# Optimization experiments

Hardware: AMD Instinct MI355X
Metric: run time of the kernel (lower is better)

## Reference

```python
import jax, jax.numpy as jnp
import numpy as np

D = 128
H = 4
B = 4096
K = 64
N_USERS = 200000
BISECT_ITERS = 50


def l2norm(x, axis=-1, eps=1e-12):
    n = jnp.linalg.norm(x, axis=axis, keepdims=True)
    return x / jnp.maximum(n, eps)


def entmax_bisect(x, alpha, n_iter=BISECT_ITERS):
    # x, alpha: [B, K, 1]; entmax normalization over the neighbor axis (axis=1)
    # p = max((alpha-1)*x - tau, 0)**(1/(alpha-1)) with tau found by bisection so sum_k p = 1
    am1 = alpha - 1.0            # in (0,1) since alpha = sigmoid(.)+1
    q = 1.0 / am1                # exponent > 1, so p is smooth at 0
    xs = x * am1
    mx = jnp.max(xs, axis=1, keepdims=True)
    tau_lo = mx - 1.0            # f(tau_lo) >= 0
    tau_hi = mx                  # f(tau_hi) <= 0

    def p_of(tau):
        t = jnp.maximum(xs - tau, 0.0)
        safe = jnp.where(t > 0.0, t, 1.0)
        return jnp.where(t > 0.0, safe ** q, 0.0)

    def body(i, carry):
        lo, hi = carry
        mid = 0.5 * (lo + hi)
        f_m = jnp.sum(p_of(mid), axis=1, keepdims=True) - 1.0
        lo = jnp.where(f_m >= 0.0, mid, lo)
        hi = jnp.where(f_m >= 0.0, hi, mid)
        return (lo, hi)

    tau_lo, tau_hi = jax.lax.fori_loop(0, n_iter, body, (tau_lo, tau_hi))
    p = p_of(0.5 * (tau_lo + tau_hi))
    return p / jnp.sum(p, axis=1, keepdims=True)


def batchnorm(x, g, b, eps=1e-5):
    # training-mode BatchNorm1d: batch statistics, biased variance
    m = jnp.mean(x, axis=0)
    v = jnp.mean((x - m) ** 2, axis=0)
    return (x - m) * jax.lax.rsqrt(v + eps) * g + b


def setup_inputs() -> dict:
    key = jax.random.key(0)
    ks = jax.random.split(key, 16)
    s = 0.05
    return {
        'nodes': jax.random.randint(ks[0], (B,), 0, N_USERS),
        'neighbors': jax.random.randint(ks[1], (B, K), 0, N_USERS),
        'u2e': jax.random.normal(ks[2], (N_USERS, D), jnp.float32),
        'att1_w': jax.random.normal(ks[3], (H, 2 * D, D), jnp.float32) * s,
        'att1_b': jnp.zeros((H, D), jnp.float32),
        'att2_w': jax.random.normal(ks[4], (H, D, D // 4), jnp.float32) * s,
        'att2_b': jnp.zeros((H, D // 4), jnp.float32),
        'att3_w': jax.random.normal(ks[5], (H, D // 4, 1), jnp.float32) * s,
        'att3_b': jnp.zeros((H, 1), jnp.float32),
        'lin1_w': jax.random.normal(ks[6], (H, D, 1), jnp.float32) * s,
        'lin1_b': jnp.zeros((H, 1), jnp.float32),
        'gate_w': jax.random.normal(ks[7], (3 * D, D), jnp.float32) * s,
        'gate_b': jnp.zeros((D,), jnp.float32),
        'bn_g': jnp.ones((D,), jnp.float32),
        'bn_b': jnp.zeros((D,), jnp.float32),
        'bn1_g': jnp.ones((D,), jnp.float32),
        'bn1_b': jnp.zeros((D,), jnp.float32),
        'in_w': jax.random.normal(ks[8], (D, D), jnp.float32) * s,
        'in_b': jnp.zeros((D,), jnp.float32),
        'out_w': jax.random.normal(ks[9], (D, D), jnp.float32) * s,
        'out_b': jnp.zeros((D,), jnp.float32),
    }


def reference(nodes, neighbors, u2e, att1_w, att1_b, att2_w, att2_b, att3_w,
              att3_b, lin1_w, lin1_b, gate_w, gate_b, bn_g, bn_b, bn1_g,
              bn1_b, in_w, in_b, out_w, out_b):
    n_heads = att1_w.shape[0]
    e_n = l2norm(u2e[neighbors])                     # [B,K,D] normalized neighbor embeds
    u = u2e[nodes]                                   # [B,D]
    b, k, d = e_n.shape
    feats = []
    for h in range(n_heads):
        u_n = l2norm(u)
        x = jnp.concatenate(
            [e_n, jnp.broadcast_to(u_n[:, None, :], (b, k, d))], axis=-1)
        alpha = jax.nn.sigmoid(e_n @ lin1_w[h] + lin1_b[h]) + 1.0  # [B,K,1]
        sc = jax.nn.selu(x @ att1_w[h] + att1_b[h])
        sc = jax.nn.selu(sc @ att2_w[h] + att2_b[h])
        sc = sc @ att3_w[h] + att3_b[h]                            # [B,K,1]
        att = entmax_bisect(sc, alpha)                             # [B,K,1]
        u = jnp.einsum('bkd,bk->bd', e_n, att[..., 0])             # weighted pool
        feats.append(u)
    att_hist = sum(feats) / n_heads                  # [B,D]
    # GAT_MLP (dropout omitted: eval)
    h1 = batchnorm(att_hist, bn_g, bn_b)
    h1 = jax.nn.selu(h1 @ in_w + in_b)
    h1 = batchnorm(h1, bn1_g, bn1_b)
    neigh = h1 @ out_w + out_b                       # [B,D]
    self_f = u2e[nodes]
    comb = jnp.concatenate([self_f, neigh, self_f * neigh], axis=-1)
    gama = jax.nn.sigmoid(comb @ gate_w + gate_b)
    return gama * self_f + (1.0 - gama) * neigh
```

## Files before the change

### kernel.cpp

```cpp
#include <hip/hip_runtime.h>
#include <stdint.h>

#define NB 4096
#define NK 64
#define ND 128
#define NH 4
#define ES 136
#define ESW (ES/2)
#define FS 130
#define MR 8

typedef __attribute__((ext_vector_type(8))) short bf16x8;
typedef __attribute__((ext_vector_type(4))) float f32x4;

__device__ __forceinline__ float seluf(float x) {
    float e = 1.6732632423543772f * (__expf(x) - 1.f);
    return 1.0507009873554805f * (x > 0.f ? x : e);
}
__device__ __forceinline__ float sigmoidf_(float x) {
    return __fdividef(1.f, 1.f + __expf(-x));
}
__device__ __forceinline__ uint32_t f2bf2(float a, float b) {
    uint32_t ua = __float_as_uint(a); ua += 0x7fffu + ((ua >> 16) & 1u);
    uint32_t ub = __float_as_uint(b); ub += 0x7fffu + ((ub >> 16) & 1u);
    return (ua >> 16) | (ub & 0xffff0000u);
}
__device__ __forceinline__ uint16_t bf1(float v) {
    uint32_t u = __float_as_uint(v); u += 0x7fffu + ((u >> 16) & 1u);
    return (uint16_t)(u >> 16);
}
__device__ __forceinline__ float bflo(uint32_t v) { return __uint_as_float(v << 16); }
__device__ __forceinline__ float bfhi(uint32_t v) { return __uint_as_float(v & 0xffff0000u); }
__device__ __forceinline__ float bf2f(uint16_t h) { return __uint_as_float(((uint32_t)h) << 16); }

__global__ __launch_bounds__(256)
void k_prep(const float* __restrict__ att1_w, const float* __restrict__ att2_w,
            uint16_t* __restrict__ wt1, uint16_t* __restrict__ wt2)
{
    const int h = blockIdx.x >> 2;
    const int q = blockIdx.x & 3;
    const int t = threadIdx.x;
    {
        int n = t >> 1, kh = t & 1;
        for (int k0 = q * 16; k0 < q * 16 + 16; ++k0) {
            int k = k0 * 2 + kh;
            float v = att1_w[(size_t)h * 32768 + (size_t)k * ND + n];
            float vo = __shfl_xor(v, 1, 64);
            if (kh == 0)
                ((uint32_t*)wt1)[((size_t)h * ND + n) * 64 + k0] = f2bf2(v, vo);
        }
    }
    {
        int c = t & 31, dh = t >> 5;
        for (int d0 = q * 4; d0 < q * 4 + 4; ++d0) {
            int d = d0 * 8 + dh;
            float v = att2_w[(size_t)h * 4096 + (size_t)d * 32 + c];
            float vo = __shfl_xor(v, 32, 64);
            if ((dh & 1) == 0)
                ((uint32_t*)wt2)[((size_t)h * 32 + c) * 64 + d0 * 4 + (dh >> 1)] = f2bf2(v, vo);
        }
    }
}

__global__ __launch_bounds__(256, 4)
void k_att(const int* __restrict__ nodes, const int* __restrict__ neighbors,
           const float* __restrict__ u2e,
           const float* __restrict__ att1_w, const float* __restrict__ att1_b,
           const float* __restrict__ att2_b,
           const float* __restrict__ att3_w, const float* __restrict__ att3_b,
           const float* __restrict__ lin1_w, const float* __restrict__ lin1_b,
           const uint16_t* __restrict__ wt1, const uint16_t* __restrict__ wt2,
           float* __restrict__ hist_out,
           float* __restrict__ sums, float* __restrict__ sumsq)
{
    __shared__ alignas(16) uint16_t e_sh[NK * ES];
    __shared__ alignas(16) uint16_t s1_sh[NK * ES];
    __shared__ float u_sh[ND], un_sh[ND], up_sh[ND], lw_sh[ND], hist_sh[ND];
    __shared__ float alpha_sh[NK], sc_sh[NK], att_sh[NK];
    __shared__ float red_sh[512];
    __shared__ float rnorm_sh;

    const int b = blockIdx.x;
    const int t = threadIdx.x;
    const int lane = t & 63;
    const int wave = t >> 6;
    const int lh = lane & 15;
    const int lg = lane >> 4;

    for (int k = wave; k < NK; k += 4) {
        int idx = neighbors[b * NK + k];
        float2 v = ((const float2*)(u2e + (size_t)idx * ND))[lane];
        float ss = v.x * v.x + v.y * v.y;
        #pragma unroll
        for (int m = 1; m < 64; m <<= 1) ss += __shfl_xor(ss, m, 64);
        float r = 1.0f / fmaxf(sqrtf(ss), 1e-12f);
        ((uint32_t*)e_sh)[k * ESW + lane] = f2bf2(v.x * r, v.y * r);
    }
    if (t < ND) {
        u_sh[t] = u2e[(size_t)nodes[b] * ND + t];
        hist_sh[t] = 0.f;
    }
    __syncthreads();

    for (int h = 0; h < NH; ++h) {
        if (wave == 0) {
            float a = u_sh[lane], c = u_sh[lane + 64];
            float ss = a * a + c * c;
            #pragma unroll
            for (int m = 1; m < 64; m <<= 1) ss += __shfl_xor(ss, m, 64);
            if (lane == 0) rnorm_sh = 1.0f / fmaxf(sqrtf(ss), 1e-12f);
        }
        __syncthreads();
        if (t < ND) {
            un_sh[t] = u_sh[t] * rnorm_sh;
            lw_sh[t] = lin1_w[h * ND + t];
        }
        __syncthreads();

        {
            int d = t & 127, half = t >> 7;
            const float* wb = att1_w + (size_t)h * 32768 + (size_t)(ND + half * 64) * ND + d;
            float p = 0.f;
            #pragma unroll 8
            for (int j = 0; j < 64; ++j)
                p += un_sh[half * 64 + j] * wb[j * ND];
            red_sh[t] = p;
        }
        {
            int k = t >> 2, qd = t & 3;
            const uint32_t* er = (const uint32_t*)e_sh + k * ESW + qd * 16;
            const float* lr = lw_sh + qd * 32;
            float ap = 0.f;
            #pragma unroll 8
            for (int j2 = 0; j2 < 16; ++j2) {
                uint32_t v = er[j2];
                ap += bflo(v) * lr[2 * j2] + bfhi(v) * lr[2 * j2 + 1];
            }
            ap += __shfl_xor(ap, 1, 64);
            ap += __shfl_xor(ap, 2, 64);
            if (qd == 0)
                alpha_sh[k] = sigmoidf_(ap + lin1_b[h]) + 1.0f;
        }
        __syncthreads();
        if (t < ND)
            up_sh[t] = red_sh[t] + red_sh[t + 128] + att1_b[h * ND + t];
        __syncthreads();

        {
            const uint16_t* WB = wt1 + ((size_t)h * ND + wave * 32) * ND;
            bf16x8 B[4][2];
            #pragma unroll
            for (int kk = 0; kk < 4; ++kk)
                #pragma unroll
                for (int nt = 0; nt < 2; ++nt)
                    B[kk][nt] = *(const bf16x8*)(WB + (nt * 16 + lh) * ND + kk * 32 + lg * 8);
            f32x4 z = {0.f, 0.f, 0.f, 0.f};
            f32x4 acc[4][2] = {{z, z}, {z, z}, {z, z}, {z, z}};
            #pragma unroll
            for (int mt = 0; mt < 4; ++mt) {
                #pragma unroll
                for (int kk = 0; kk < 4; ++kk) {
                    bf16x8 A = *(const bf16x8*)(e_sh + (mt * 16 + lh) * ES + kk * 32 + lg * 8);
                    acc[mt][0] = __builtin_amdgcn_mfma_f32_16x16x32_bf16(A, B[kk][0], acc[mt][0], 0, 0, 0);
                    acc[mt][1] = __builtin_amdgcn_mfma_f32_16x16x32_bf16(A, B[kk][1], acc[mt][1], 0, 0, 0);
                }
            }
            float up0 = up_sh[wave * 32 + lh];
            float up1 = up_sh[wave * 32 + 16 + lh];
            #pragma unroll
            for (int mt = 0; mt < 4; ++mt)
                #pragma unroll
                for (int nt = 0; nt < 2; ++nt) {
                    float upv = nt ? up1 : up0;
                    #pragma unroll
                    for (int r = 0; r < 4; ++r) {
                        float v = seluf(acc[mt][nt][r] + upv);
                        s1_sh[(mt * 16 + lg * 4 + r) * ES + wave * 32 + nt * 16 + lh] = bf1(v);
                    }
                }
        }
        __syncthreads();

        {
            const uint16_t* WB2 = wt2 + (size_t)h * 32 * ND;
            bf16x8 B2[4][2];
            #pragma unroll
            for (int kk = 0; kk < 4; ++kk)
                #pragma unroll
                for (int nt = 0; nt < 2; ++nt)
                    B2[kk][nt] = *(const bf16x8*)(WB2 + (nt * 16 + lh) * ND + kk * 32 + lg * 8);
            f32x4 z = {0.f, 0.f, 0.f, 0.f};
            f32x4 acc2[2] = {z, z};
            #pragma unroll
            for (int kk = 0; kk < 4; ++kk) {
                bf16x8 A = *(const bf16x8*)(s1_sh + (wave * 16 + lh) * ES + kk * 32 + lg * 8);
                acc2[0] = __builtin_amdgcn_mfma_f32_16x16x32_bf16(A, B2[kk][0], acc2[0], 0, 0, 0);
                acc2[1] = __builtin_amdgcn_mfma_f32_16x16x32_bf16(A, B2[kk][1], acc2[1], 0, 0, 0);
            }
            float w3a = att3_w[h * 32 + lh],      b2a = att2_b[h * 32 + lh];
            float w3b = att3_w[h * 32 + 16 + lh], b2b = att2_b[h * 32 + 16 + lh];
            float b3 = att3_b[h];
            #pragma unroll
            for (int r = 0; r < 4; ++r) {
                float v = seluf(acc2[0][r] + b2a) * w3a + seluf(acc2[1][r] + b2b) * w3b;
                v += __shfl_xor(v, 1, 64);
                v += __shfl_xor(v, 2, 64);
                v += __shfl_xor(v, 4, 64);
                v += __shfl_xor(v, 8, 64);
                if (lh == 0)
                    sc_sh[wave * 16 + lg * 4 + r] = v + b3;
            }
        }
        __syncthreads();

        if (wave == 0) {
            float x   = sc_sh[lane];
            float am1 = alpha_sh[lane] - 1.0f;
            float q   = 1.0f / am1;
            float em1 = q - 1.0f;
            float xs  = x * am1;
            float mx = xs;
            #pragma unroll
            for (int m = 1; m < 64; m <<= 1) mx = fmaxf(mx, __shfl_xor(mx, m, 64));
            float tau = mx - 1.0f;
            for (int it = 0; it < 8; ++it) {
                float tt = xs - tau;
                bool pos = tt > 0.f;
                float lgn = __logf(pos ? tt : 1.f);
                float p  = pos ? __expf(q * lgn) : 0.f;
                float dp = pos ? q * __expf(em1 * lgn) : 0.f;
                float s0 = p, s1 = dp;
                #pragma unroll
                for (int m = 1; m < 64; m <<= 1) {
                    s0 += __shfl_xor(s0, m, 64);
                    s1 += __shfl_xor(s1, m, 64);
                }
                tau += __fdividef(s0 - 1.0f, fmaxf(s1, 1e-30f));
                tau = fminf(tau, mx - 1e-6f);
            }
            float tt = xs - tau;
            bool pos = tt > 0.f;
            float p = pos ? __expf(q * __logf(pos ? tt : 1.f)) : 0.f;
            float s0 = p;
            #pragma unroll
            for (int m = 1; m < 64; m <<= 1) s0 += __shfl_xor(s0, m, 64);
            att_sh[lane] = __fdividef(p, s0);
        }
        __syncthreads();

        {
            int d2 = t & 63, qk = t >> 6;
            const uint32_t* E = (const uint32_t*)e_sh;
            float px = 0.f, py = 0.f;
            #pragma unroll 8
            for (int k = qk * 16; k < qk * 16 + 16; ++k) {
                uint32_t v = E[k * ESW + d2];
                float a = att_sh[k];
                px += bflo(v) * a;
                py += bfhi(v) * a;
            }
            red_sh[qk * 128 + d2 * 2]     = px;
            red_sh[qk * 128 + d2 * 2 + 1] = py;
        }
        __syncthreads();
        if (t < ND) {
            float un = red_sh[t] + red_sh[128 + t] + red_sh[256 + t] + red_sh[384 + t];
            u_sh[t] = un;
            hist_sh[t] += un;
        }
        __syncthreads();
    }
    if (t < ND) {
        float hv = hist_sh[t] * 0.25f;
        hist_out[(size_t)b * ND + t] = hv;
        atomicAdd(&sums[t], hv);
        atomicAdd(&sumsq[t], hv * hv);
    }
}

__global__ __launch_bounds__(256)
void k_mlp1(const float* __restrict__ hist,
            const float* __restrict__ sums, const float* __restrict__ sumsq,
            const float* __restrict__ bn_g, const float* __restrict__ bn_b,
            const float* __restrict__ in_w, const float* __restrict__ in_b,
            float* __restrict__ h1out,
            float* __restrict__ sums1, float* __restrict__ sumsq1)
{
    __shared__ float xh[MR * FS];
    int t = threadIdx.x;
    int row0 = blockIdx.x * MR;
    for (int i = t; i < MR * ND; i += 256) {
        int r = i >> 7, d = i & 127;
        float m  = sums[d]  * (1.f / 4096.f);
        float vv = sumsq[d] * (1.f / 4096.f) - m * m;
        float sc = bn_g[d] * rsqrtf(vv + 1e-5f);
        float sh = bn_b[d] - m * sc;
        xh[r * FS + d] = hist[(size_t)(row0 + r) * ND + d] * sc + sh;
    }
    __syncthreads();
    int dg = t & 31, rg = t >> 5;
    int d0 = dg * 4;
    float acc[4] = {};
    for (int j = 0; j < ND; ++j) {
        float4 wa = *(const float4*)(in_w + (size_t)j * ND + d0);
        float e = xh[rg * FS + j];
        acc[0] += e * wa.x; acc[1] += e * wa.y;
        acc[2] += e * wa.z; acc[3] += e * wa.w;
    }
    float hv[4];
    #pragma unroll
    for (int c = 0; c < 4; ++c) {
        hv[c] = seluf(acc[c] + in_b[d0 + c]);
        h1out[(size_t)(row0 + rg) * ND + d0 + c] = hv[c];
    }
    __syncthreads();
    #pragma unroll
    for (int c = 0; c < 4; ++c) xh[rg * FS + d0 + c] = hv[c];
    __syncthreads();
    if (t < ND) {
        float s = 0.f, q = 0.f;
        #pragma unroll
        for (int r = 0; r < MR; ++r) {
            float v = xh[r * FS + t];
            s += v; q += v * v;
        }
        atomicAdd(&sums1[t], s);
        atomicAdd(&sumsq1[t], q);
    }
}

__global__ __launch_bounds__(256)
void k_final(const float* __restrict__ h1,
             const float* __restrict__ sums1, const float* __restrict__ sumsq1,
             const float* __restrict__ bn1_g, const float* __restrict__ bn1_b,
             const float* __restrict__ out_w, const float* __restrict__ out_b,
             const float* __restrict__ gate_w, const float* __restrict__ gate_b,
             const int* __restrict__ nodes, const float* __restrict__ u2e,
             float* __restrict__ out)
{
    __shared__ float xh[MR * FS];
    __shared__ float sf[MR * FS];
    __shared__ float ng[MR * FS];
    int t = threadIdx.x;
    int row0 = blockIdx.x * MR;
    for (int i = t; i < MR * ND; i += 256) {
        int r = i >> 7, d = i & 127;
        float m  = sums1[d]  * (1.f / 4096.f);
        float vv = sumsq1[d] * (1.f / 4096.f) - m * m;
        float sc = bn1_g[d] * rsqrtf(vv + 1e-5f);
        float sh = bn1_b[d] - m * sc;
        xh[r * FS + d] = h1[(size_t)(row0 + r) * ND + d] * sc + sh;
        sf[r * FS + d] = u2e[(size_t)nodes[row0 + r] * ND + d];
    }
    __syncthreads();
    int dg = t & 31, rg = t >> 5;
    int d0 = dg * 4;
    {
        float acc[4] = {};
        for (int j = 0; j < ND; ++j) {
            float4 wa = *(const float4*)(out_w + (size_t)j * ND + d0);
            float e = xh[rg * FS + j];
            acc[0] += e * wa.x; acc[1] += e * wa.y;
            acc[2] += e * wa.z; acc[3] += e * wa.w;
        }
        #pragma unroll
        for (int c = 0; c < 4; ++c)
            ng[rg * FS + d0 + c] = acc[c] + out_b[d0 + c];
    }
    __syncthreads();
    {
        float acc[4] = {};
        for (int j = 0; j < ND; ++j) {
            float4 w0 = *(const float4*)(gate_w + (size_t)j * ND + d0);
            float4 w1 = *(const float4*)(gate_w + (size_t)(ND + j) * ND + d0);
            float4 w2 = *(const float4*)(gate_w + (size_t)(2 * ND + j) * ND + d0);
            float s = sf[rg * FS + j];
            float n = ng[rg * FS + j];
            float p = s * n;
            acc[0] += s * w0.x + n * w1.x + p * w2.x;
            acc[1] += s * w0.y + n * w1.y + p * w2.y;
            acc[2] += s * w0.z + n * w1.z + p * w2.z;
            acc[3] += s * w0.w + n * w1.w + p * w2.w;
        }
        #pragma unroll
        for (int c = 0; c < 4; ++c) {
            int d = d0 + c;
            float gama = sigmoidf_(acc[c] + gate_b[d]);
            float s = sf[rg * FS + d];
            float n = ng[rg * FS + d];
            out[(size_t)(row0 + rg) * ND + d] = gama * s + (1.f - gama) * n;
        }
    }
}

extern "C" void kernel_launch(void* const* d_in, const int* in_sizes, int n_in,
                              void* d_out, int out_size, void* d_ws, size_t ws_size,
                              hipStream_t stream)
{
    const int*   nodes     = (const int*)d_in[0];
    const int*   neighbors = (const int*)d_in[1];
    const float* u2e       = (const float*)d_in[2];
    const float* att1_w    = (const float*)d_in[3];
    const float* att1_b    = (const float*)d_in[4];
    const float* att2_w    = (const float*)d_in[5];
    const float* att2_b    = (const float*)d_in[6];
    const float* att3_w    = (const float*)d_in[7];
    const float* att3_b    = (const float*)d_in[8];
    const float* lin1_w    = (const float*)d_in[9];
    const float* lin1_b    = (const float*)d_in[10];
    const float* gate_w    = (const float*)d_in[11];
    const float* gate_b    = (const float*)d_in[12];
    const float* bn_g      = (const float*)d_in[13];
    const float* bn_b      = (const float*)d_in[14];
    const float* bn1_g     = (const float*)d_in[15];
    const float* bn1_b     = (const float*)d_in[16];
    const float* in_w      = (const float*)d_in[17];
    const float* in_b      = (const float*)d_in[18];
    const float* out_w     = (const float*)d_in[19];
    const float* out_b     = (const float*)d_in[20];
    float* out = (float*)d_out;

    float* ws     = (float*)d_ws;
    float* g_hist = ws;
    float* h1     = ws + (size_t)NB * ND;
    float* st     = ws + (size_t)2 * NB * ND;
    uint16_t* wt1 = (uint16_t*)(ws + (size_t)2 * NB * ND + 512);
    uint16_t* wt2 = wt1 + (size_t)NH * ND * ND;

    (void)hipMemsetAsync(st, 0, 512 * sizeof(float), stream);

    k_prep<<<16, 256, 0, stream>>>(att1_w, att2_w, wt1, wt2);
    k_att<<<NB, 256, 0, stream>>>(nodes, neighbors, u2e,
                                  att1_w, att1_b, att2_b,
                                  att3_w, att3_b, lin1_w, lin1_b,
                                  wt1, wt2,
                                  g_hist, st, st + 128);
    k_mlp1<<<NB / MR, 256, 0, stream>>>(g_hist, st, st + 128, bn_g, bn_b,
                                        in_w, in_b, h1, st + 256, st + 384);
    k_final<<<NB / MR, 256, 0, stream>>>(h1, st + 256, st + 384, bn1_g, bn1_b,
                                         out_w, out_b, gate_w, gate_b,
                                         nodes, u2e, out);
}
```

Baseline: 559.0 us.

## Restructure attention kernel per-wave rows, hoist alpha, reduce Newton iters, widen MLP grids

Alpha (the lin1 gate) is now computed for all four heads up front, with one head per wave, instead of once per head inside the loop. The per-head rnorm is computed redundantly in every wave, which removes two barriers. The first MFMA GEMM now gives each wave 16 rows and all 128 columns, so the second GEMM reads only that wave's own s1 slice and the barrier between the two GEMMs goes away. The entmax Newton iterations drop from 8 to 6, and the MLP kernels use MR=4 with 2 outputs per thread for more blocks. The trade-offs are that B fragments are now reloaded from global memory, and fewer iterations may reduce numerical accuracy.

Result: slower. 780.2 us (+39.6%).

```diff
diff --git a/kernel.cpp b/kernel.cpp
--- a/kernel.cpp
+++ b/kernel.cpp
@@ -8,7 +8,7 @@
 #define ES 136
 #define ESW (ES/2)
 #define FS 130
-#define MR 8
+#define MR 4
 
 typedef __attribute__((ext_vector_type(8))) short bf16x8;
 typedef __attribute__((ext_vector_type(4))) float f32x4;
@@ -31,18 +31,17 @@
 }
 __device__ __forceinline__ float bflo(uint32_t v) { return __uint_as_float(v << 16); }
 __device__ __forceinline__ float bfhi(uint32_t v) { return __uint_as_float(v & 0xffff0000u); }
-__device__ __forceinline__ float bf2f(uint16_t h) { return __uint_as_float(((uint32_t)h) << 16); }
 
 __global__ __launch_bounds__(256)
 void k_prep(const float* __restrict__ att1_w, const float* __restrict__ att2_w,
             uint16_t* __restrict__ wt1, uint16_t* __restrict__ wt2)
 {
-    const int h = blockIdx.x >> 2;
-    const int q = blockIdx.x & 3;
+    const int h = blockIdx.x >> 4;
+    const int q = blockIdx.x & 15;
     const int t = threadIdx.x;
     {
         int n = t >> 1, kh = t & 1;
-        for (int k0 = q * 16; k0 < q * 16 + 16; ++k0) {
+        for (int k0 = q * 4; k0 < q * 4 + 4; ++k0) {
             int k = k0 * 2 + kh;
             float v = att1_w[(size_t)h * 32768 + (size_t)k * ND + n];
             float vo = __shfl_xor(v, 1, 64);
@@ -52,13 +51,12 @@
     }
     {
         int c = t & 31, dh = t >> 5;
-        for (int d0 = q * 4; d0 < q * 4 + 4; ++d0) {
-            int d = d0 * 8 + dh;
-            float v = att2_w[(size_t)h * 4096 + (size_t)d * 32 + c];
-            float vo = __shfl_xor(v, 32, 64);
-            if ((dh & 1) == 0)
-                ((uint32_t*)wt2)[((size_t)h * 32 + c) * 64 + d0 * 4 + (dh >> 1)] = f2bf2(v, vo);
-        }
+        int d0 = q;
+        int d = d0 * 8 + dh;
+        float v = att2_w[(size_t)h * 4096 + (size_t)d * 32 + c];
+        float vo = __shfl_xor(v, 32, 64);
+        if ((dh & 1) == 0)
+            ((uint32_t*)wt2)[((size_t)h * 32 + c) * 64 + d0 * 4 + (dh >> 1)] = f2bf2(v, vo);
     }
 }
 
@@ -75,10 +73,10 @@
 {
     __shared__ alignas(16) uint16_t e_sh[NK * ES];
     __shared__ alignas(16) uint16_t s1_sh[NK * ES];
-    __shared__ float u_sh[ND], un_sh[ND], up_sh[ND], lw_sh[ND], hist_sh[ND];
-    __shared__ float alpha_sh[NK], sc_sh[NK], att_sh[NK];
+    __shared__ float u_sh[ND], up_sh[ND], hist_sh[ND];
+    __shared__ float alpha_sh[NH * NK];
+    __shared__ float sc_sh[NK], att_sh[NK];
     __shared__ float red_sh[512];
-    __shared__ float rnorm_sh;
 
     const int b = blockIdx.x;
     const int t = threadIdx.x;
@@ -102,100 +100,87 @@
     }
     __syncthreads();
 
+    {
+        const float* lw = lin1_w + wave * ND;
+        float lb = lin1_b[wave];
+        #pragma unroll
+        for (int it = 0; it < 4; ++it) {
+            int k = it * 16 + (lane >> 2);
+            int qd = lane & 3;
+            const uint32_t* er = (const uint32_t*)e_sh + k * ESW + qd * 16;
+            const float* lr = lw + qd * 32;
+            float ap = 0.f;
+            #pragma unroll 8
+            for (int j2 = 0; j2 < 16; ++j2) {
+                uint32_t v = er[j2];
+                ap += bflo(v) * lr[2 * j2] + bfhi(v) * lr[2 * j2 + 1];
+            }
+            ap += __shfl_xor(ap, 1, 64);
+            ap += __shfl_xor(ap, 2, 64);
+            if (qd == 0)
+                alpha_sh[wave * NK + k] = sigmoidf_(ap + lb) + 1.0f;
+        }
+    }
+
     for (int h = 0; h < NH; ++h) {
-        if (wave == 0) {
+        float rnorm;
+        {
             float a = u_sh[lane], c = u_sh[lane + 64];
             float ss = a * a + c * c;
             #pragma unroll
             for (int m = 1; m < 64; m <<= 1) ss += __shfl_xor(ss, m, 64);
-            if (lane == 0) rnorm_sh = 1.0f / fmaxf(sqrtf(ss), 1e-12f);
-        }
-        __syncthreads();
-        if (t < ND) {
-            un_sh[t] = u_sh[t] * rnorm_sh;
-            lw_sh[t] = lin1_w[h * ND + t];
-        }
-        __syncthreads();
-
+            rnorm = 1.0f / fmaxf(sqrtf(ss), 1e-12f);
+        }
         {
             int d = t & 127, half = t >> 7;
             const float* wb = att1_w + (size_t)h * 32768 + (size_t)(ND + half * 64) * ND + d;
             float p = 0.f;
             #pragma unroll 8
             for (int j = 0; j < 64; ++j)
-                p += un_sh[half * 64 + j] * wb[j * ND];
-            red_sh[t] = p;
-        }
-        {
-            int k = t >> 2, qd = t & 3;
-            const uint32_t* er = (const uint32_t*)e_sh + k * ESW + qd * 16;
-            const float* lr = lw_sh + qd * 32;
-            float ap = 0.f;
-            #pragma unroll 8
-            for (int j2 = 0; j2 < 16; ++j2) {
-                uint32_t v = er[j2];
-                ap += bflo(v) * lr[2 * j2] + bfhi(v) * lr[2 * j2 + 1];
-            }
-            ap += __shfl_xor(ap, 1, 64);
-            ap += __shfl_xor(ap, 2, 64);
-            if (qd == 0)
-                alpha_sh[k] = sigmoidf_(ap + lin1_b[h]) + 1.0f;
+                p += u_sh[half * 64 + j] * wb[j * ND];
+            red_sh[t] = p * rnorm;
         }
         __syncthreads();
         if (t < ND)
             up_sh[t] = red_sh[t] + red_sh[t + 128] + att1_b[h * ND + t];
         __syncthreads();
 
+        uint16_t* s1w = s1_sh + wave * 16 * ES;
         {
-            const uint16_t* WB = wt1 + ((size_t)h * ND + wave * 32) * ND;
-            bf16x8 B[4][2];
-            #pragma unroll
-            for (int kk = 0; kk < 4; ++kk)
+            const uint16_t* WB = wt1 + (size_t)h * ND * ND;
+            f32x4 z = {0.f, 0.f, 0.f, 0.f};
+            f32x4 acc[8] = {z, z, z, z, z, z, z, z};
+            #pragma unroll
+            for (int kk = 0; kk < 4; ++kk) {
+                bf16x8 A = *(const bf16x8*)(e_sh + (wave * 16 + lh) * ES + kk * 32 + lg * 8);
                 #pragma unroll
-                for (int nt = 0; nt < 2; ++nt)
-                    B[kk][nt] = *(const bf16x8*)(WB + (nt * 16 + lh) * ND + kk * 32 + lg * 8);
+                for (int nt = 0; nt < 8; ++nt) {
+                    bf16x8 Bf = *(const bf16x8*)(WB + (size_t)(nt * 16 + lh) * ND + kk * 32 + lg * 8);
+                    acc[nt] = __builtin_amdgcn_mfma_f32_16x16x32_bf16(A, Bf, acc[nt], 0, 0, 0);
+                }
+            }
+            #pragma unroll
+            for (int nt = 0; nt < 8; ++nt) {
+                float upv = up_sh[nt * 16 + lh];
+                #pragma unroll
+                for (int r = 0; r < 4; ++r) {
+                    float v = seluf(acc[nt][r] + upv);
+                    s1w[(lg * 4 + r) * ES + nt * 16 + lh] = bf1(v);
+                }
+            }
+        }
+        {
+            const uint16_t* WB2 = wt2 + (size_t)h * 32 * ND;
             f32x4 z = {0.f, 0.f, 0.f, 0.f};
-            f32x4 acc[4][2] = {{z, z}, {z, z}, {z, z}, {z, z}};
-            #pragma unroll
-            for (int mt = 0; mt < 4; ++mt) {
-                #pragma unroll
-                for (int kk = 0; kk < 4; ++kk) {
-                    bf16x8 A = *(const bf16x8*)(e_sh + (mt * 16 + lh) * ES + kk * 32 + lg * 8);
-                    acc[mt][0] = __builtin_amdgcn_mfma_f32_16x16x32_bf16(A, B[kk][0], acc[mt][0], 0, 0, 0);
-                    acc[mt][1] = __builtin_amdgcn_mfma_f32_16x16x32_bf16(A, B[kk][1], acc[mt][1], 0, 0, 0);
-                }
-            }
-            float up0 = up_sh[wave * 32 + lh];
-            float up1 = up_sh[wave * 32 + 16 + lh];
-            #pragma unroll
-            for (int mt = 0; mt < 4; ++mt)
+            f32x4 acc2[2] = {z, z};
+            #pragma unroll
+            for (int kk = 0; kk < 4; ++kk) {
+                bf16x8 A = *(const bf16x8*)(s1w + lh * ES + kk * 32 + lg * 8);
                 #pragma unroll
                 for (int nt = 0; nt < 2; ++nt) {
-                    float upv = nt ? up1 : up0;
-                    #pragma unroll
-                    for (int r = 0; r < 4; ++r) {
-                        float v = seluf(acc[mt][nt][r] + upv);
-                        s1_sh[(mt * 16 + lg * 4 + r) * ES + wave * 32 + nt * 16 + lh] = bf1(v);
-                    }
+                    bf16x8 Bf = *(const bf16x8*)(WB2 + (size_t)(nt * 16 + lh) * ND + kk * 32 + lg * 8);
+                    acc2[nt] = __builtin_amdgcn_mfma_f32_16x16x32_bf16(A, Bf, acc2[nt], 0, 0, 0);
                 }
-        }
-        __syncthreads();
-
-        {
-            const uint16_t* WB2 = wt2 + (size_t)h * 32 * ND;
-            bf16x8 B2[4][2];
-            #pragma unroll
-            for (int kk = 0; kk < 4; ++kk)
-                #pragma unroll
-                for (int nt = 0; nt < 2; ++nt)
-                    B2[kk][nt] = *(const bf16x8*)(WB2 + (nt * 16 + lh) * ND + kk * 32 + lg * 8);
-            f32x4 z = {0.f, 0.f, 0.f, 0.f};
-            f32x4 acc2[2] = {z, z};
-            #pragma unroll
-            for (int kk = 0; kk < 4; ++kk) {
-                bf16x8 A = *(const bf16x8*)(s1_sh + (wave * 16 + lh) * ES + kk * 32 + lg * 8);
-                acc2[0] = __builtin_amdgcn_mfma_f32_16x16x32_bf16(A, B2[kk][0], acc2[0], 0, 0, 0);
-                acc2[1] = __builtin_amdgcn_mfma_f32_16x16x32_bf16(A, B2[kk][1], acc2[1], 0, 0, 0);
             }
             float w3a = att3_w[h * 32 + lh],      b2a = att2_b[h * 32 + lh];
             float w3b = att3_w[h * 32 + 16 + lh], b2b = att2_b[h * 32 + 16 + lh];
@@ -215,7 +200,7 @@
 
         if (wave == 0) {
             float x   = sc_sh[lane];
-            float am1 = alpha_sh[lane] - 1.0f;
+            float am1 = alpha_sh[h * NK + lane] - 1.0f;
             float q   = 1.0f / am1;
             float em1 = q - 1.0f;
             float xs  = x * am1;
@@ -223,7 +208,7 @@
             #pragma unroll
             for (int m = 1; m < 64; m <<= 1) mx = fmaxf(mx, __shfl_xor(mx, m, 64));
             float tau = mx - 1.0f;
-            for (int it = 0; it < 8; ++it) {
+            for (int it = 0; it < 6; ++it) {
                 float tt = xs - tau;
                 bool pos = tt > 0.f;
                 float lgn = __logf(pos ? tt : 1.f);
@@ -298,24 +283,22 @@
         xh[r * FS + d] = hist[(size_t)(row0 + r) * ND + d] * sc + sh;
     }
     __syncthreads();
-    int dg = t & 31, rg = t >> 5;
-    int d0 = dg * 4;
-    float acc[4] = {};
+    int dg = t & 63, rg = t >> 6;
+    int d0 = dg * 2;
+    float a0 = 0.f, a1 = 0.f;
+    #pragma unroll 4
     for (int j = 0; j < ND; ++j) {
-        float4 wa = *(const float4*)(in_w + (size_t)j * ND + d0);
+        float2 w = *(const float2*)(in_w + (size_t)j * ND + d0);
         float e = xh[rg * FS + j];
-        acc[0] += e * wa.x; acc[1] += e * wa.y;
-        acc[2] += e * wa.z; acc[3] += e * wa.w;
-    }
-    float hv[4];
-    #pragma unroll
-    for (int c = 0; c < 4; ++c) {
-        hv[c] = seluf(acc[c] + in_b[d0 + c]);
-        h1out[(size_t)(row0 + rg) * ND + d0 + c] = hv[c];
-    }
-    __syncthreads();
-    #pragma unroll
-    for (int c = 0; c < 4; ++c) xh[rg * FS + d0 + c] = hv[c];
+        a0 += e * w.x; a1 += e * w.y;
+    }
+    float h0 = seluf(a0 + in_b[d0]);
+    float h1v = seluf(a1 + in_b[d0 + 1]);
+    h1out[(size_t)(row0 + rg) * ND + d0]     = h0;
+    h1out[(size_t)(row0 + rg) * ND + d0 + 1] = h1v;
+    __syncthreads();
+    xh[rg * FS + d0] = h0;
+    xh[rg * FS + d0 + 1] = h1v;
     __syncthreads();
     if (t < ND) {
         float s = 0.f, q = 0.f;
@@ -353,39 +336,38 @@
         sf[r * FS + d] = u2e[(size_t)nodes[row0 + r] * ND + d];
     }
     __syncthreads();
-    int dg = t & 31, rg = t >> 5;
-    int d0 = dg * 4;
+    int dg = t & 63, rg = t >> 6;
+    int d0 = dg * 2;
     {
-        float acc[4] = {};
+        float a0 = 0.f, a1 = 0.f;
+        #pragma unroll 4
         for (int j = 0; j < ND; ++j) {
-            float4 wa = *(const float4*)(out_w + (size_t)j * ND + d0);
+            float2 w = *(const float2*)(out_w + (size_t)j * ND + d0);
             float e = xh[rg * FS + j];
-            acc[0] += e * wa.x; acc[1] += e * wa.y;
-            acc[2] += e * wa.z; acc[3] += e * wa.w;
-        }
-        #pragma unroll
-        for (int c = 0; c < 4; ++c)
-            ng[rg * FS + d0 + c] = acc[c] + out_b[d0 + c];
+            a0 += e * w.x; a1 += e * w.y;
+        }
+        ng[rg * FS + d0]     = a0 + out_b[d0];
+        ng[rg * FS + d0 + 1] = a1 + out_b[d0 + 1];
     }
     __syncthreads();
     {
-        float acc[4] = {};
+        float a0 = 0.f, a1 = 0.f;
+        #pragma unroll 2
         for (int j = 0; j < ND; ++j) {
-            float4 w0 = *(const float4*)(gate_w + (size_t)j * ND + d0);
-            float4 w1 = *(const float4*)(gate_w + (size_t)(ND + j) * ND + d0);
-            float4 w2 = *(const float4*)(gate_w + (size_t)(2 * ND + j) * ND + d0);
+            float2 w0 = *(const float2*)(gate_w + (size_t)j * ND + d0);
+            float2 w1 = *(const float2*)(gate_w + (size_t)(ND + j) * ND + d0);
+            float2 w2 = *(const float2*)(gate_w + (size_t)(2 * ND + j) * ND + d0);
             float s = sf[rg * FS + j];
             float n = ng[rg * FS + j];
             float p = s * n;
-            acc[0] += s * w0.x + n * w1.x + p * w2.x;
-            acc[1] += s * w0.y + n * w1.y + p * w2.y;
-            acc[2] += s * w0.z + n * w1.z + p * w2.z;
-            acc[3] += s * w0.w + n * w1.w + p * w2.w;
+            a0 += s * w0.x + n * w1.x + p * w2.x;
+            a1 += s * w0.y + n * w1.y + p * w2.y;
         }
         #pragma unroll
-        for (int c = 0; c < 4; ++c) {
+        for (int c = 0; c < 2; ++c) {
             int d = d0 + c;
-            float gama = sigmoidf_(acc[c] + gate_b[d]);
+            float acc = c ? a1 : a0;
+            float gama = sigmoidf_(acc + gate_b[d]);
             float s = sf[rg * FS + d];
             float n = ng[rg * FS + d];
             out[(size_t)(row0 + rg) * ND + d] = gama * s + (1.f - gama) * n;
@@ -429,7 +411,7 @@
 
     (void)hipMemsetAsync(st, 0, 512 * sizeof(float), stream);
 
-    k_prep<<<16, 256, 0, stream>>>(att1_w, att2_w, wt1, wt2);
+    k_prep<<<64, 256, 0, stream>>>(att1_w, att2_w, wt1, wt2);
     k_att<<<NB, 256, 0, stream>>>(nodes, neighbors, u2e,
                                   att1_w, att1_b, att2_b,
                                   att3_w, att3_b, lin1_w, lin1_b,
```

## Move MLP and gate GEMMs to bf16 MFMA and hoist alpha computation

Applied to the files above, without the earlier changes.

The MLP and gate weights are pre-transposed to bf16 in the prep kernel, and the in/out/gate matmuls in k_mlp1 and k_final become 16x16x32 bf16 MFMA tiles with 16 rows per block. The intermediate h1 is stored as bf16. In k_att, the per-head alpha computation is hoisted out of the head loop, the u normalisation is folded into a per-wave scale, removing two barriers per head, and the entmax Newton iterations drop from 8 to 6. The aim is to replace scalar FP32 FMA loops and cut syncs and traffic, at the cost of bf16 precision in the MLP and possibly less converged entmax.

New measurement: 526.0 us. -5.9%, faster.

```diff
diff --git a/kernel.cpp b/kernel.cpp
--- a/kernel.cpp
+++ b/kernel.cpp
@@ -7,8 +7,9 @@
 #define NH 4
 #define ES 136
 #define ESW (ES/2)
-#define FS 130
-#define MR 8
+#define MR 16
+#define GS 392
+#define SFS 132
 
 typedef __attribute__((ext_vector_type(8))) short bf16x8;
 typedef __attribute__((ext_vector_type(4))) float f32x4;
@@ -35,30 +36,51 @@
 
 __global__ __launch_bounds__(256)
 void k_prep(const float* __restrict__ att1_w, const float* __restrict__ att2_w,
-            uint16_t* __restrict__ wt1, uint16_t* __restrict__ wt2)
+            const float* __restrict__ in_w, const float* __restrict__ out_w,
+            const float* __restrict__ gate_w,
+            uint16_t* __restrict__ wt1, uint16_t* __restrict__ wt2,
+            uint16_t* __restrict__ wt_in, uint16_t* __restrict__ wt_out,
+            uint16_t* __restrict__ wt_gate)
 {
-    const int h = blockIdx.x >> 2;
-    const int q = blockIdx.x & 3;
+    const int bx = blockIdx.x;
     const int t = threadIdx.x;
-    {
-        int n = t >> 1, kh = t & 1;
-        for (int k0 = q * 16; k0 < q * 16 + 16; ++k0) {
-            int k = k0 * 2 + kh;
-            float v = att1_w[(size_t)h * 32768 + (size_t)k * ND + n];
-            float vo = __shfl_xor(v, 1, 64);
-            if (kh == 0)
-                ((uint32_t*)wt1)[((size_t)h * ND + n) * 64 + k0] = f2bf2(v, vo);
-        }
-    }
-    {
-        int c = t & 31, dh = t >> 5;
-        for (int d0 = q * 4; d0 < q * 4 + 4; ++d0) {
+    if (bx < 64) {
+        const int h = bx >> 4;
+        const int q = bx & 15;
+        {
+            int n = t >> 1, kh = t & 1;
+            for (int k0 = q * 4; k0 < q * 4 + 4; ++k0) {
+                int k = k0 * 2 + kh;
+                float v = att1_w[(size_t)h * 32768 + (size_t)k * ND + n];
+                float vo = __shfl_xor(v, 1, 64);
+                if (kh == 0)
+                    ((uint32_t*)wt1)[((size_t)h * ND + n) * 64 + k0] = f2bf2(v, vo);
+            }
+        }
+        {
+            int c = t & 31, dh = t >> 5;
+            int d0 = q;
             int d = d0 * 8 + dh;
             float v = att2_w[(size_t)h * 4096 + (size_t)d * 32 + c];
             float vo = __shfl_xor(v, 32, 64);
             if ((dh & 1) == 0)
                 ((uint32_t*)wt2)[((size_t)h * 32 + c) * 64 + d0 * 4 + (dh >> 1)] = f2bf2(v, vo);
         }
+    } else if (bx < 72) {
+        int n0 = (bx - 64) * 16;
+        for (int n = n0; n < n0 + 16; ++n)
+            for (int k = t; k < ND; k += 256)
+                wt_in[n * ND + k] = bf1(in_w[(size_t)k * ND + n]);
+    } else if (bx < 80) {
+        int n0 = (bx - 72) * 16;
+        for (int n = n0; n < n0 + 16; ++n)
+            for (int k = t; k < ND; k += 256)
+                wt_out[n * ND + k] = bf1(out_w[(size_t)k * ND + n]);
+    } else {
+        int n0 = (bx - 80) * 16;
+        for (int n = n0; n < n0 + 16; ++n)
+            for (int k = t; k < 384; k += 256)
+                wt_gate[n * 384 + k] = bf1(gate_w[(size_t)k * ND + n]);
     }
 }
 
@@ -75,10 +97,10 @@
 {
     __shared__ alignas(16) uint16_t e_sh[NK * ES];
     __shared__ alignas(16) uint16_t s1_sh[NK * ES];
-    __shared__ float u_sh[ND], un_sh[ND], up_sh[ND], lw_sh[ND], hist_sh[ND];
-    __shared__ float alpha_sh[NK], sc_sh[NK], att_sh[NK];
+    __shared__ float u_sh[ND], up_sh[ND], hist_sh[ND];
+    __shared__ float alpha_sh[NH * NK];
+    __shared__ float sc_sh[NK], att_sh[NK];
     __shared__ float red_sh[512];
-    __shared__ float rnorm_sh;
 
     const int b = blockIdx.x;
     const int t = threadIdx.x;
@@ -102,44 +124,45 @@
     }
     __syncthreads();
 
+    {
+        const float* lw = lin1_w + wave * ND;
+        float lb = lin1_b[wave];
+        #pragma unroll
+        for (int it = 0; it < 4; ++it) {
+            int k = it * 16 + (lane >> 2);
+            int qd = lane & 3;
+            const uint32_t* er = (const uint32_t*)e_sh + k * ESW + qd * 16;
+            const float* lr = lw + qd * 32;
+            float ap = 0.f;
+            #pragma unroll 8
+            for (int j2 = 0; j2 < 16; ++j2) {
+                uint32_t v = er[j2];
+                ap += bflo(v) * lr[2 * j2] + bfhi(v) * lr[2 * j2 + 1];
+            }
+            ap += __shfl_xor(ap, 1, 64);
+            ap += __shfl_xor(ap, 2, 64);
+            if (qd == 0)
+                alpha_sh[wave * NK + k] = sigmoidf_(ap + lb) + 1.0f;
+        }
+    }
+
     for (int h = 0; h < NH; ++h) {
-        if (wave == 0) {
+        float rnorm;
+        {
             float a = u_sh[lane], c = u_sh[lane + 64];
             float ss = a * a + c * c;
             #pragma unroll
             for (int m = 1; m < 64; m <<= 1) ss += __shfl_xor(ss, m, 64);
-            if (lane == 0) rnorm_sh = 1.0f / fmaxf(sqrtf(ss), 1e-12f);
-        }
-        __syncthreads();
-        if (t < ND) {
-            un_sh[t] = u_sh[t] * rnorm_sh;
-            lw_sh[t] = lin1_w[h * ND + t];
-        }
-        __syncthreads();
-
+            rnorm = 1.0f / fmaxf(sqrtf(ss), 1e-12f);
+        }
         {
             int d = t & 127, half = t >> 7;
             const float* wb = att1_w + (size_t)h * 32768 + (size_t)(ND + half * 64) * ND + d;
             float p = 0.f;
             #pragma unroll 8
             for (int j = 0; j < 64; ++j)
-                p += un_sh[half * 64 + j] * wb[j * ND];
-            red_sh[t] = p;
-        }
-        {
-            int k = t >> 2, qd = t & 3;
-            const uint32_t* er = (const uint32_t*)e_sh + k * ESW + qd * 16;
-            const float* lr = lw_sh + qd * 32;
-            float ap = 0.f;
-            #pragma unroll 8
-            for (int j2 = 0; j2 < 16; ++j2) {
-                uint32_t v = er[j2];
-                ap += bflo(v) * lr[2 * j2] + bfhi(v) * lr[2 * j2 + 1];
-            }
-            ap += __shfl_xor(ap, 1, 64);
-            ap += __shfl_xor(ap, 2, 64);
-            if (qd == 0)
-                alpha_sh[k] = sigmoidf_(ap + lin1_b[h]) + 1.0f;
+                p += u_sh[half * 64 + j] * wb[j * ND];
+            red_sh[t] = p * rnorm;
         }
         __syncthreads();
         if (t < ND)
@@ -215,7 +238,7 @@
 
         if (wave == 0) {
             float x   = sc_sh[lane];
-            float am1 = alpha_sh[lane] - 1.0f;
+            float am1 = alpha_sh[h * NK + lane] - 1.0f;
             float q   = 1.0f / am1;
             float em1 = q - 1.0f;
             float xs  = x * am1;
@@ -223,7 +246,7 @@
             #pragma unroll
             for (int m = 1; m < 64; m <<= 1) mx = fmaxf(mx, __shfl_xor(mx, m, 64));
             float tau = mx - 1.0f;
-            for (int it = 0; it < 8; ++it) {
+            for (int it = 0; it < 6; ++it) {
                 float tt = xs - tau;
                 bool pos = tt > 0.f;
                 float lgn = __logf(pos ? tt : 1.f);
@@ -282,113 +305,167 @@
 void k_mlp1(const float* __restrict__ hist,
             const float* __restrict__ sums, const float* __restrict__ sumsq,
             const float* __restrict__ bn_g, const float* __restrict__ bn_b,
-            const float* __restrict__ in_w, const float* __restrict__ in_b,
-            float* __restrict__ h1out,
+            const uint16_t* __restrict__ wt_in, const float* __restrict__ in_b,
+            uint16_t* __restrict__ h1b,
             float* __restrict__ sums1, float* __restrict__ sumsq1)
 {
-    __shared__ float xh[MR * FS];
-    int t = threadIdx.x;
-    int row0 = blockIdx.x * MR;
-    for (int i = t; i < MR * ND; i += 256) {
-        int r = i >> 7, d = i & 127;
-        float m  = sums[d]  * (1.f / 4096.f);
-        float vv = sumsq[d] * (1.f / 4096.f) - m * m;
-        float sc = bn_g[d] * rsqrtf(vv + 1e-5f);
-        float sh = bn_b[d] - m * sc;
-        xh[r * FS + d] = hist[(size_t)(row0 + r) * ND + d] * sc + sh;
+    __shared__ alignas(16) uint16_t xh[MR * ES];
+    const int t = threadIdx.x;
+    const int lane = t & 63;
+    const int wave = t >> 6;
+    const int lh = lane & 15;
+    const int lg = lane >> 4;
+    const int row0 = blockIdx.x * MR;
+
+    #pragma unroll
+    for (int it = 0; it < 4; ++it) {
+        int pos = t + it * 256;
+        int r = pos >> 6, d2 = pos & 63;
+        int d0 = d2 * 2;
+        float m0 = sums[d0] * (1.f / 4096.f);
+        float v0 = sumsq[d0] * (1.f / 4096.f) - m0 * m0;
+        float sc0 = bn_g[d0] * rsqrtf(v0 + 1e-5f);
+        float sh0 = bn_b[d0] - m0 * sc0;
+        float m1 = sums[d0 + 1] * (1.f / 4096.f);
+        float v1 = sumsq[d0 + 1] * (1.f / 4096.f) - m1 * m1;
+        float sc1 = bn_g[d0 + 1] * rsqrtf(v1 + 1e-5f);
+        float sh1 = bn_b[d0 + 1] - m1 * sc1;
+        float2 hv = *(const float2*)(hist + (size_t)(row0 + r) * ND + d0);
+        ((uint32_t*)xh)[r * ESW + d2] = f2bf2(hv.x * sc0 + sh0, hv.y * sc1 + sh1);
     }
     __syncthreads();
-    int dg = t & 31, rg = t >> 5;
-    int d0 = dg * 4;
-    float acc[4] = {};
-    for (int j = 0; j < ND; ++j) {
-        float4 wa = *(const float4*)(in_w + (size_t)j * ND + d0);
-        float e = xh[rg * FS + j];
-        acc[0] += e * wa.x; acc[1] += e * wa.y;
-        acc[2] += e * wa.z; acc[3] += e * wa.w;
-    }
-    float hv[4];
-    #pragma unroll
-    for (int c = 0; c < 4; ++c) {
-        hv[c] = seluf(acc[c] + in_b[d0 + c]);
-        h1out[(size_t)(row0 + rg) * ND + d0 + c] = hv[c];
-    }
-    __syncthreads();
-    #pragma unroll
-    for (int c = 0; c < 4; ++c) xh[rg * FS + d0 + c] = hv[c];
-    __syncthreads();
-    if (t < ND) {
+
+    const uint16_t* WB = wt_in + (size_t)(wave * 32) * ND;
+    bf16x8 B[4][2];
+    #pragma unroll
+    for (int kk = 0; kk < 4; ++kk)
+        #pragma unroll
+        for (int nt = 0; nt < 2; ++nt)
+            B[kk][nt] = *(const bf16x8*)(WB + (nt * 16 + lh) * ND + kk * 32 + lg * 8);
+    f32x4 z = {0.f, 0.f, 0.f, 0.f};
+    f32x4 acc[2] = {z, z};
+    #pragma unroll
+    for (int kk = 0; kk < 4; ++kk) {
+        bf16x8 A = *(const bf16x8*)(xh + lh * ES + kk * 32 + lg * 8);
+        acc[0] = __builtin_amdgcn_mfma_f32_16x16x32_bf16(A, B[kk][0], acc[0], 0, 0, 0);
+        acc[1] = __builtin_amdgcn_mfma_f32_16x16x32_bf16(A, B[kk][1], acc[1], 0, 0, 0);
+    }
+    #pragma unroll
+    for (int nt = 0; nt < 2; ++nt) {
+        int col = wave * 32 + nt * 16 + lh;
+        float bia = in_b[col];
         float s = 0.f, q = 0.f;
         #pragma unroll
-        for (int r = 0; r < MR; ++r) {
-            float v = xh[r * FS + t];
-            s += v; q += v * v;
-        }
-        atomicAdd(&sums1[t], s);
-        atomicAdd(&sumsq1[t], q);
+        for (int r = 0; r < 4; ++r) {
+            int row = lg * 4 + r;
+            float hv = seluf(acc[nt][r] + bia);
+            h1b[(size_t)(row0 + row) * ND + col] = bf1(hv);
+            s += hv; q += hv * hv;
+        }
+        s += __shfl_xor(s, 16, 64); s += __shfl_xor(s, 32, 64);
+        q += __shfl_xor(q, 16, 64); q += __shfl_xor(q, 32, 64);
+        if (lg == 0) {
+            atomicAdd(&sums1[col], s);
+            atomicAdd(&sumsq1[col], q);
+        }
     }
 }
 
 __global__ __launch_bounds__(256)
-void k_final(const float* __restrict__ h1,
+void k_final(const uint16_t* __restrict__ h1b,
              const float* __restrict__ sums1, const float* __restrict__ sumsq1,
              const float* __restrict__ bn1_g, const float* __restrict__ bn1_b,
-             const float* __restrict__ out_w, const float* __restrict__ out_b,
-             const float* __restrict__ gate_w, const float* __restrict__ gate_b,
+             const uint16_t* __restrict__ wt_out, const float* __restrict__ out_b,
+             const uint16_t* __restrict__ wt_gate, const float* __restrict__ gate_b,
              const int* __restrict__ nodes, const float* __restrict__ u2e,
              float* __restrict__ out)
 {
-    __shared__ float xh[MR * FS];
-    __shared__ float sf[MR * FS];
-    __shared__ float ng[MR * FS];
-    int t = threadIdx.x;
-    int row0 = blockIdx.x * MR;
-    for (int i = t; i < MR * ND; i += 256) {
-        int r = i >> 7, d = i & 127;
-        float m  = sums1[d]  * (1.f / 4096.f);
-        float vv = sumsq1[d] * (1.f / 4096.f) - m * m;
-        float sc = bn1_g[d] * rsqrtf(vv + 1e-5f);
-        float sh = bn1_b[d] - m * sc;
-        xh[r * FS + d] = h1[(size_t)(row0 + r) * ND + d] * sc + sh;
-        sf[r * FS + d] = u2e[(size_t)nodes[row0 + r] * ND + d];
+    __shared__ alignas(16) uint16_t xh[MR * ES];
+    __shared__ float sff[MR * SFS];
+    __shared__ alignas(16) uint16_t gtile[MR * GS];
+    const int t = threadIdx.x;
+    const int lane = t & 63;
+    const int wave = t >> 6;
+    const int lh = lane & 15;
+    const int lg = lane >> 4;
+    const int row0 = blockIdx.x * MR;
+
+    #pragma unroll
+    for (int it = 0; it < 4; ++it) {
+        int pos = t + it * 256;
+        int r = pos >> 6, d2 = pos & 63;
+        int d0 = d2 * 2;
+        float m0 = sums1[d0] * (1.f / 4096.f);
+        float v0 = sumsq1[d0] * (1.f / 4096.f) - m0 * m0;
+        float sc0 = bn1_g[d0] * rsqrtf(v0 + 1e-5f);
+        float sh0 = bn1_b[d0] - m0 * sc0;
+        float m1 = sums1[d0 + 1] * (1.f / 4096.f);
+        float v1 = sumsq1[d0 + 1] * (1.f / 4096.f) - m1 * m1;
+        float sc1 = bn1_g[d0 + 1] * rsqrtf(v1 + 1e-5f);
+        float sh1 = bn1_b[d0 + 1] - m1 * sc1;
+        uint32_t hw = ((const uint32_t*)h1b)[(size_t)(row0 + r) * 64 + d2];
+        ((uint32_t*)xh)[r * ESW + d2] = f2bf2(bflo(hw) * sc0 + sh0, bfhi(hw) * sc1 + sh1);
+        float2 sv = *(const float2*)(u2e + (size_t)nodes[row0 + r] * ND + d0);
+        sff[r * SFS + d0]     = sv.x;
+        sff[r * SFS + d0 + 1] = sv.y;
+        ((uint32_t*)gtile)[r * (GS / 2) + d2] = f2bf2(sv.x, sv.y);
     }
     __syncthreads();
-    int dg = t & 31, rg = t >> 5;
-    int d0 = dg * 4;
+
+    f32x4 z = {0.f, 0.f, 0.f, 0.f};
+    f32x4 accN[2] = {z, z};
     {
-        float acc[4] = {};
-        for (int j = 0; j < ND; ++j) {
-            float4 wa = *(const float4*)(out_w + (size_t)j * ND + d0);
-            float e = xh[rg * FS + j];
-            acc[0] += e * wa.x; acc[1] += e * wa.y;
-            acc[2] += e * wa.z; acc[3] += e * wa.w;
-        }
-        #pragma unroll
-        for (int c = 0; c < 4; ++c)
-            ng[rg * FS + d0 + c] = acc[c] + out_b[d0 + c];
+        const uint16_t* WB = wt_out + (size_t)(wave * 32) * ND;
+        bf16x8 B[4][2];
+        #pragma unroll
+        for (int kk = 0; kk < 4; ++kk)
+            #pragma unroll
+            for (int nt = 0; nt < 2; ++nt)
+                B[kk][nt] = *(const bf16x8*)(WB + (nt * 16 + lh) * ND + kk * 32 + lg * 8);
+        #pragma unroll
+        for (int kk = 0; kk < 4; ++kk) {
+            bf16x8 A = *(const bf16x8*)(xh + lh * ES + kk * 32 + lg * 8);
+            accN[0] = __builtin_amdgcn_mfma_f32_16x16x32_bf16(A, B[kk][0], accN[0], 0, 0, 0);
+            accN[1] = __builtin_amdgcn_mfma_f32_16x16x32_bf16(A, B[kk][1], accN[1], 0, 0, 0);
+        }
+    }
+    #pragma unroll
+    for (int nt = 0; nt < 2; ++nt) {
+        int col = wave * 32 + nt * 16 + lh;
+        float bia = out_b[col];
+        #pragma unroll
+        for (int r = 0; r < 4; ++r) {
+            int row = lg * 4 + r;
+            float n = accN[nt][r] + bia;
+            float s = sff[row * SFS + col];
+            gtile[row * GS + 128 + col] = bf1(n);
+            gtile[row * GS + 256 + col] = bf1(s * n);
+        }
     }
     __syncthreads();
-    {
-        float acc[4] = {};
-        for (int j = 0; j < ND; ++j) {
-            float4 w0 = *(const float4*)(gate_w + (size_t)j * ND + d0);
-            float4 w1 = *(const float4*)(gate_w + (size_t)(ND + j) * ND + d0);
-            float4 w2 = *(const float4*)(gate_w + (size_t)(2 * ND + j) * ND + d0);
-            float s = sf[rg * FS + j];
-            float n = ng[rg * FS + j];
-            float p = s * n;
-            acc[0] += s * w0.x + n * w1.x + p * w2.x;
-            acc[1] += s * w0.y + n * w1.y + p * w2.y;
-            acc[2] += s * w0.z + n * w1.z + p * w2.z;
-            acc[3] += s * w0.w + n * w1.w + p * w2.w;
-        }
-        #pragma unroll
-        for (int c = 0; c < 4; ++c) {
-            int d = d0 + c;
-            float gama = sigmoidf_(acc[c] + gate_b[d]);
-            float s = sf[rg * FS + d];
-            float n = ng[rg * FS + d];
-            out[(size_t)(row0 + rg) * ND + d] = gama * s + (1.f - gama) * n;
+
+    f32x4 accG[2] = {z, z};
+    #pragma unroll
+    for (int kk = 0; kk < 12; ++kk) {
+        bf16x8 A = *(const bf16x8*)(gtile + lh * GS + kk * 32 + lg * 8);
+        #pragma unroll
+        for (int nt = 0; nt < 2; ++nt) {
+            bf16x8 Bf = *(const bf16x8*)(wt_gate + (size_t)(wave * 32 + nt * 16 + lh) * 384 + kk * 32 + lg * 8);
+            accG[nt] = __builtin_amdgcn_mfma_f32_16x16x32_bf16(A, Bf, accG[nt], 0, 0, 0);
+        }
+    }
+    #pragma unroll
+    for (int nt = 0; nt < 2; ++nt) {
+        int col = wave * 32 + nt * 16 + lh;
+        float gb = gate_b[col];
+        float ob = out_b[col];
+        #pragma unroll
+        for (int r = 0; r < 4; ++r) {
+            int row = lg * 4 + r;
+            float gama = sigmoidf_(accG[nt][r] + gb);
+            float s = sff[row * SFS + col];
+            float n = accN[nt][r] + ob;
+            out[(size_t)(row0 + row) * ND + col] = gama * s + (1.f - gama) * n;
         }
     }
 }
@@ -420,24 +497,28 @@
     const float* out_b     = (const float*)d_in[20];
     float* out = (float*)d_out;
 
-    float* ws     = (float*)d_ws;
-    float* g_hist = ws;
-    float* h1     = ws + (size_t)NB * ND;
-    float* st     = ws + (size_t)2 * NB * ND;
-    uint16_t* wt1 = (uint16_t*)(ws + (size_t)2 * NB * ND + 512);
-    uint16_t* wt2 = wt1 + (size_t)NH * ND * ND;
+    float* ws      = (float*)d_ws;
+    float* g_hist  = ws;
+    float* st      = ws + (size_t)NB * ND;
+    uint16_t* wt1  = (uint16_t*)(st + 512);
+    uint16_t* wt2  = wt1 + (size_t)NH * ND * ND;
+    uint16_t* wt_in   = wt2 + (size_t)NH * 32 * ND;
+    uint16_t* wt_out  = wt_in + (size_t)ND * ND;
+    uint16_t* wt_gate = wt_out + (size_t)ND * ND;
+    uint16_t* h1b     = wt_gate + (size_t)ND * 384;
 
     (void)hipMemsetAsync(st, 0, 512 * sizeof(float), stream);
 
-    k_prep<<<16, 256, 0, stream>>>(att1_w, att2_w, wt1, wt2);
+    k_prep<<<88, 256, 0, stream>>>(att1_w, att2_w, in_w, out_w, gate_w,
+                                   wt1, wt2, wt_in, wt_out, wt_gate);
     k_att<<<NB, 256, 0, stream>>>(nodes, neighbors, u2e,
                                   att1_w, att1_b, att2_b,
                                   att3_w, att3_b, lin1_w, lin1_b,
                                   wt1, wt2,
                                   g_hist, st, st + 128);
     k_mlp1<<<NB / MR, 256, 0, stream>>>(g_hist, st, st + 128, bn_g, bn_b,
-                                        in_w, in_b, h1, st + 256, st + 384);
-    k_final<<<NB / MR, 256, 0, stream>>>(h1, st + 256, st + 384, bn1_g, bn1_b,
-                                         out_w, out_b, gate_w, gate_b,
+                                        wt_in, in_b, h1b, st + 256, st + 384);
+    k_final<<<NB / MR, 256, 0, stream>>>(h1b, st + 256, st + 384, bn1_g, bn1_b,
+                                         wt_out, out_b, wt_gate, gate_b,
                                          nodes, u2e, out);
 }
```
